# Optimization experiments

Measured on AMD Instinct MI355X. Metric: run time of the kernel, lower is better.

Reference implementation:

```python
import jax, jax.numpy as jnp
import numpy as np

NUM_USERS = 100000
NUM_ITEMS = 50000
EMBED_DIM = 64
NUM_LAYERS = 3
NNZ = 4800000  # 2 * num_interactions (symmetric bipartite adjacency)


def setup_inputs() -> dict:
    key = jax.random.key(0)
    k_u, k_i, k_r, k_c, k_v = jax.random.split(key, 5)
    N = NUM_USERS + NUM_ITEMS
    E = NNZ // 2
    # Xavier-uniform-style embeddings (any float init is fine for a math reference)
    user_emb = jax.random.normal(k_u, (NUM_USERS, EMBED_DIM), dtype=jnp.float32) * 0.1
    item_emb = jax.random.normal(k_i, (NUM_ITEMS, EMBED_DIM), dtype=jnp.float32) * 0.1
    # Build a symmetric bipartite COO adjacency: user->item and item->user edges.
    u = jax.random.randint(k_r, (E,), 0, NUM_USERS, dtype=jnp.int32)
    i = jax.random.randint(k_c, (E,), NUM_USERS, N, dtype=jnp.int32)
    adj_rows = jnp.concatenate([u, i])
    adj_cols = jnp.concatenate([i, u])
    # Normalized adjacency values (D^-1/2 A D^-1/2 in real LightGCN); random positive here.
    v = jax.random.uniform(k_v, (E,), dtype=jnp.float32, minval=0.01, maxval=0.1)
    adj_vals = jnp.concatenate([v, v])
    return {"user_emb": user_emb, "item_emb": item_emb, "adj_vals": adj_vals,
            "adj_rows": adj_rows, "adj_cols": adj_cols}


def reference(user_emb, item_emb, adj_vals, adj_rows, adj_cols):
    num_users = user_emb.shape[0]
    N = num_users + item_emb.shape[0]
    ego = jnp.concatenate([user_emb, item_emb], axis=0)  # [N, D]
    x = ego
    acc = ego  # running sum across layers (fused layer-mean)
    for _ in range(NUM_LAYERS):
        # SpMM: gather source embeddings, scale by edge value, scatter-add to rows.
        x = jax.ops.segment_sum(adj_vals[:, None] * x[adj_cols], adj_rows,
                                num_segments=N)
        acc = acc + x
    final = acc / jnp.asarray(NUM_LAYERS + 1, dtype=ego.dtype)
    return final[:num_users], final[num_users:]
```

## Files before the change

### kernel.cpp

```cpp
#include <hip/hip_runtime.h>

static constexpr int NUSERS = 100000;
static constexpr int NITEMS = 50000;
static constexpr int NNODES = NUSERS + NITEMS;
static constexpr int D      = 64;
static constexpr int NNZE   = 4800000;
static constexpr int NVEC4  = NNODES * D / 4;
static constexpr int NU4    = NUSERS * D / 4;

static constexpr int NB       = 512;
static constexpr int RPB      = (NNODES + NB - 1) / NB;
static constexpr int CHUNK    = 4096;
static constexpr int P1_BLOCKS = (NNZE + CHUNK - 1) / CHUNK;

__device__ __forceinline__ unsigned bf16rne(float f) {
    unsigned u = __float_as_uint(f);
    return (u + 0x7FFFu + ((u >> 16) & 1u)) >> 16;
}
__device__ __forceinline__ float bflo(unsigned u) { return __uint_as_float(u << 16); }
__device__ __forceinline__ float bfhi(unsigned u) { return __uint_as_float(u & 0xFFFF0000u); }

__global__ void lg_init(const float4* __restrict__ ue, const float4* __restrict__ ie,
                        uint2* __restrict__ x) {
    int stride = gridDim.x * blockDim.x;
    for (int i = blockIdx.x * blockDim.x + threadIdx.x; i < NVEC4; i += stride) {
        float4 v = (i < NU4) ? ue[i] : ie[i - NU4];
        x[i] = make_uint2(bf16rne(v.x) | (bf16rne(v.y) << 16),
                          bf16rne(v.z) | (bf16rne(v.w) << 16));
    }
}

__global__ void __launch_bounds__(512)
lg_bcnt(const int* __restrict__ rows, int* __restrict__ bucketCnt) {
    __shared__ int cnt[NB];
    int t = threadIdx.x;
    cnt[t] = 0;
    __syncthreads();
    int c0 = blockIdx.x * CHUNK;
    int c1 = min(c0 + CHUNK, NNZE);
    #pragma unroll
    for (int pass = 0; pass < 2; ++pass) {
        int e = c0 + (pass * 512 + t) * 4;
        if (e < c1) {
            int4 r4 = *(const int4*)(rows + e);
            atomicAdd(&cnt[r4.x / RPB], 1);
            atomicAdd(&cnt[r4.y / RPB], 1);
            atomicAdd(&cnt[r4.z / RPB], 1);
            atomicAdd(&cnt[r4.w / RPB], 1);
        }
    }
    __syncthreads();
    int n = cnt[t];
    if (n) atomicAdd(&bucketCnt[t], n);
}

__global__ void __launch_bounds__(512)
lg_bscan(const int* __restrict__ bucketCnt, int* __restrict__ bbase,
         int* __restrict__ gcur) {
    __shared__ int s[NB];
    int t = threadIdx.x;
    int v = bucketCnt[t];
    s[t] = v;
    __syncthreads();
    for (int off = 1; off < NB; off <<= 1) {
        int tmp = (t >= off) ? s[t - off] : 0;
        __syncthreads();
        s[t] += tmp;
        __syncthreads();
    }
    int ex = s[t] - v;
    bbase[t] = ex;
    gcur[t] = ex;
    if (t == NB - 1) bbase[NB] = s[t];
}

__global__ void __launch_bounds__(512)
lg_part1(const int* __restrict__ rows, const int* __restrict__ cols,
         const float* __restrict__ vals, int* __restrict__ gcur,
         int2* __restrict__ stage) {
    __shared__ int s_cnt[NB];
    __shared__ int s_lcur[NB];
    __shared__ int s_gofs[NB];
    __shared__ int2 s_pay[CHUNK];
    __shared__ unsigned short s_bid[CHUNK];
    int t = threadIdx.x;
    int c0 = blockIdx.x * CHUNK;
    int c1 = min(c0 + CHUNK, NNZE);
    s_cnt[t] = 0;
    __syncthreads();

    int  eb[8], ep[8]; float ev[8];
    bool has0, has1;
    {
        int e = c0 + t * 4;
        has0 = e < c1;
        if (has0) {
            int4 r4 = *(const int4*)(rows + e);
            int4 c4 = *(const int4*)(cols + e);
            float4 v4 = *(const float4*)(vals + e);
            eb[0] = r4.x / RPB; ep[0] = c4.x | ((r4.x - eb[0] * RPB) << 18); ev[0] = v4.x;
            eb[1] = r4.y / RPB; ep[1] = c4.y | ((r4.y - eb[1] * RPB) << 18); ev[1] = v4.y;
            eb[2] = r4.z / RPB; ep[2] = c4.z | ((r4.z - eb[2] * RPB) << 18); ev[2] = v4.z;
            eb[3] = r4.w / RPB; ep[3] = c4.w | ((r4.w - eb[3] * RPB) << 18); ev[3] = v4.w;
            atomicAdd(&s_cnt[eb[0]], 1); atomicAdd(&s_cnt[eb[1]], 1);
            atomicAdd(&s_cnt[eb[2]], 1); atomicAdd(&s_cnt[eb[3]], 1);
        }
        e = c0 + (512 + t) * 4;
        has1 = e < c1;
        if (has1) {
            int4 r4 = *(const int4*)(rows + e);
            int4 c4 = *(const int4*)(cols + e);
            float4 v4 = *(const float4*)(vals + e);
            eb[4] = r4.x / RPB; ep[4] = c4.x | ((r4.x - eb[4] * RPB) << 18); ev[4] = v4.x;
            eb[5] = r4.y / RPB; ep[5] = c4.y | ((r4.y - eb[5] * RPB) << 18); ev[5] = v4.y;
            eb[6] = r4.z / RPB; ep[6] = c4.z | ((r4.z - eb[6] * RPB) << 18); ev[6] = v4.z;
            eb[7] = r4.w / RPB; ep[7] = c4.w | ((r4.w - eb[7] * RPB) << 18); ev[7] = v4.w;
            atomicAdd(&s_cnt[eb[4]], 1); atomicAdd(&s_cnt[eb[5]], 1);
            atomicAdd(&s_cnt[eb[6]], 1); atomicAdd(&s_cnt[eb[7]], 1);
        }
    }
    __syncthreads();

    int myCnt = s_cnt[t];
    for (int off = 1; off < NB; off <<= 1) {
        int tmp = (t >= off) ? s_cnt[t - off] : 0;
        __syncthreads();
        s_cnt[t] += tmp;
        __syncthreads();
    }
    int lstart = s_cnt[t] - myCnt;
    int gbase = myCnt ? atomicAdd(&gcur[t], myCnt) : 0;
    s_lcur[t] = lstart;
    s_gofs[t] = gbase - lstart;
    __syncthreads();

    #pragma unroll
    for (int k = 0; k < 4; ++k) {
        if (has0) {
            int pos = atomicAdd(&s_lcur[eb[k]], 1);
            s_pay[pos] = make_int2(ep[k], __float_as_int(ev[k]));
            s_bid[pos] = (unsigned short)eb[k];
        }
    }
    #pragma unroll
    for (int k = 4; k < 8; ++k) {
        if (has1) {
            int pos = atomicAdd(&s_lcur[eb[k]], 1);
            s_pay[pos] = make_int2(ep[k], __float_as_int(ev[k]));
            s_bid[pos] = (unsigned short)eb[k];
        }
    }
    __syncthreads();

    int n = c1 - c0;
    for (int p = t; p < n; p += 512) {
        int b = s_bid[p];
        stage[s_gofs[b] + p] = s_pay[p];
    }
}

__global__ void __launch_bounds__(512)
lg_part2(const int* __restrict__ bbase, const int2* __restrict__ stage,
         int2* __restrict__ csr, int* __restrict__ rowptr) {
    __shared__ int s[NB];
    __shared__ int lcur[RPB];
    int b = blockIdx.x;
    int t = threadIdx.x;
    int r0 = b * RPB;
    int nrows = min(RPB, NNODES - r0);
    int s0 = bbase[b], s1 = bbase[b + 1];

    s[t] = 0;
    __syncthreads();
    for (int p = s0 + t; p < s1; p += 512)
        atomicAdd(&s[(stage[p].x >> 18) & 511], 1);
    __syncthreads();
    int v = s[t];
    for (int off = 1; off < NB; off <<= 1) {
        int tmp = (t >= off) ? s[t - off] : 0;
        __syncthreads();
        s[t] += tmp;
        __syncthreads();
    }
    int pos0 = s0 + s[t] - v;
    if (t < nrows) {
        rowptr[r0 + t] = pos0;
        lcur[t] = pos0;
    }
    if (b == gridDim.x - 1 && t == 0) rowptr[NNODES] = NNZE;
    __syncthreads();
    for (int p = s0 + t; p < s1; p += 512) {
        int2 cv = stage[p];
        int rl = (cv.x >> 18) & 511;
        int pos = atomicAdd(&lcur[rl], 1);
        csr[pos] = make_int2(cv.x & 0x3FFFF, cv.y);
    }
}

__global__ void __launch_bounds__(256)
lg_spmm(const int* __restrict__ rowptr, const int2* __restrict__ csr,
        const uint2* __restrict__ x, uint2* __restrict__ y) {
    int lane16 = threadIdx.x & 15;
    int r = (blockIdx.x * blockDim.x + threadIdx.x) >> 4;
    if (r >= NNODES) return;
    int p0 = rowptr[r], p1 = rowptr[r + 1];
    float4 acc = {0.f, 0.f, 0.f, 0.f};
    int p = p0;
    for (; p + 4 <= p1; p += 4) {
        int2 cv0 = csr[p], cv1 = csr[p + 1], cv2 = csr[p + 2], cv3 = csr[p + 3];
        uint2 x0 = x[cv0.x * 16 + lane16];
        uint2 x1 = x[cv1.x * 16 + lane16];
        uint2 x2 = x[cv2.x * 16 + lane16];
        uint2 x3 = x[cv3.x * 16 + lane16];
        float v0 = __int_as_float(cv0.y), v1 = __int_as_float(cv1.y);
        float v2 = __int_as_float(cv2.y), v3 = __int_as_float(cv3.y);
        acc.x += v0 * bflo(x0.x) + v1 * bflo(x1.x) + v2 * bflo(x2.x) + v3 * bflo(x3.x);
        acc.y += v0 * bfhi(x0.x) + v1 * bfhi(x1.x) + v2 * bfhi(x2.x) + v3 * bfhi(x3.x);
        acc.z += v0 * bflo(x0.y) + v1 * bflo(x1.y) + v2 * bflo(x2.y) + v3 * bflo(x3.y);
        acc.w += v0 * bfhi(x0.y) + v1 * bfhi(x1.y) + v2 * bfhi(x2.y) + v3 * bfhi(x3.y);
    }
    for (; p < p1; ++p) {
        int2 cv = csr[p];
        uint2 xv = x[cv.x * 16 + lane16];
        float v = __int_as_float(cv.y);
        acc.x += v * bflo(xv.x); acc.y += v * bfhi(xv.x);
        acc.z += v * bflo(xv.y); acc.w += v * bfhi(xv.y);
    }
    y[r * 16 + lane16] = make_uint2(bf16rne(acc.x) | (bf16rne(acc.y) << 16),
                                    bf16rne(acc.z) | (bf16rne(acc.w) << 16));
}

__global__ void lg_combine(const float4* __restrict__ ue, const float4* __restrict__ ie,
                           const uint2* __restrict__ y1, const uint2* __restrict__ y2,
                           const uint2* __restrict__ y3, float4* __restrict__ out) {
    int stride = gridDim.x * blockDim.x;
    for (int i = blockIdx.x * blockDim.x + threadIdx.x; i < NVEC4; i += stride) {
        float4 e = (i < NU4) ? ue[i] : ie[i - NU4];
        uint2 a = y1[i], b = y2[i], c = y3[i];
        float4 o;
        o.x = (e.x + bflo(a.x) + bflo(b.x) + bflo(c.x)) * 0.25f;
        o.y = (e.y + bfhi(a.x) + bfhi(b.x) + bfhi(c.x)) * 0.25f;
        o.z = (e.z + bflo(a.y) + bflo(b.y) + bflo(c.y)) * 0.25f;
        o.w = (e.w + bfhi(a.y) + bfhi(b.y) + bfhi(c.y)) * 0.25f;
        out[i] = o;
    }
}

extern "C" void kernel_launch(void* const* d_in, const int* in_sizes, int n_in,
                              void* d_out, int out_size, void* d_ws, size_t ws_size,
                              hipStream_t stream) {
    const float* ue   = (const float*)d_in[0];
    const float* ie   = (const float*)d_in[1];
    const float* vals = (const float*)d_in[2];
    const int*   rows = (const int*)d_in[3];
    const int*   cols = (const int*)d_in[4];
    float* out = (float*)d_out;

    uint2* xa     = (uint2*)d_ws;
    uint2* xb     = xa + NVEC4;
    int2*  csr    = (int2*)(xb + NVEC4);
    int2*  stage  = csr + NNZE;
    uint2* y3     = (uint2*)stage;
    int*   rowptr = (int*)(stage + NNZE);
    int*   bucketCnt = rowptr + (NNODES + 1);
    int*   bbase  = bucketCnt + NB;
    int*   gcur   = bbase + (NB + 1);

    const int spmmBlocks = NNODES * 16 / 256;

    lg_init<<<2048, 256, 0, stream>>>((const float4*)ue, (const float4*)ie, xa);
    hipMemsetAsync(bucketCnt, 0, NB * sizeof(int), stream);
    lg_bcnt<<<P1_BLOCKS, 512, 0, stream>>>(rows, bucketCnt);
    lg_bscan<<<1, NB, 0, stream>>>(bucketCnt, bbase, gcur);
    lg_part1<<<P1_BLOCKS, 512, 0, stream>>>(rows, cols, vals, gcur, stage);
    lg_part2<<<NB, 512, 0, stream>>>(bbase, stage, csr, rowptr);

    lg_spmm<<<spmmBlocks, 256, 0, stream>>>(rowptr, csr, xa, xb);
    lg_spmm<<<spmmBlocks, 256, 0, stream>>>(rowptr, csr, xb, xa);
    lg_spmm<<<spmmBlocks, 256, 0, stream>>>(rowptr, csr, xa, y3);

    lg_combine<<<2048, 256, 0, stream>>>((const float4*)ue, (const float4*)ie,
                                         xb, xa, y3, (float4*)out);
}
```

Measured before the change: 373.5 us.

## Split CSR into separate column and bf16 value arrays, unroll SpMM by eight

Edge values are rounded to bf16 during partitioning and stored as 16-bit values. The interleaved int2 staging and CSR arrays become a struct-of-arrays pair: a 4-byte column array and a 2-byte value array. This cuts per-edge metadata traffic from 8 to 6 bytes in the partition, sort and all three SpMM passes. The SpMM inner loop is also unrolled to 8 edges to keep more gathers in flight. The cost is extra precision loss on the adjacency weights and more separate loads per edge.

```diff
diff --git a/kernel.cpp b/kernel.cpp
--- a/kernel.cpp
+++ b/kernel.cpp
@@ -77,11 +77,12 @@
 __global__ void __launch_bounds__(512)
 lg_part1(const int* __restrict__ rows, const int* __restrict__ cols,
          const float* __restrict__ vals, int* __restrict__ gcur,
-         int2* __restrict__ stage) {
+         int* __restrict__ stagec, unsigned short* __restrict__ stagev) {
     __shared__ int s_cnt[NB];
     __shared__ int s_lcur[NB];
     __shared__ int s_gofs[NB];
-    __shared__ int2 s_pay[CHUNK];
+    __shared__ int s_payc[CHUNK];
+    __shared__ unsigned short s_payv[CHUNK];
     __shared__ unsigned short s_bid[CHUNK];
     int t = threadIdx.x;
     int c0 = blockIdx.x * CHUNK;
@@ -89,7 +90,7 @@
     s_cnt[t] = 0;
     __syncthreads();
 
-    int  eb[8], ep[8]; float ev[8];
+    int  eb[8], ep[8]; unsigned short ev[8];
     bool has0, has1;
     {
         int e = c0 + t * 4;
@@ -98,10 +99,10 @@
             int4 r4 = *(const int4*)(rows + e);
             int4 c4 = *(const int4*)(cols + e);
             float4 v4 = *(const float4*)(vals + e);
-            eb[0] = r4.x / RPB; ep[0] = c4.x | ((r4.x - eb[0] * RPB) << 18); ev[0] = v4.x;
-            eb[1] = r4.y / RPB; ep[1] = c4.y | ((r4.y - eb[1] * RPB) << 18); ev[1] = v4.y;
-            eb[2] = r4.z / RPB; ep[2] = c4.z | ((r4.z - eb[2] * RPB) << 18); ev[2] = v4.z;
-            eb[3] = r4.w / RPB; ep[3] = c4.w | ((r4.w - eb[3] * RPB) << 18); ev[3] = v4.w;
+            eb[0] = r4.x / RPB; ep[0] = c4.x | ((r4.x - eb[0] * RPB) << 18); ev[0] = (unsigned short)bf16rne(v4.x);
+            eb[1] = r4.y / RPB; ep[1] = c4.y | ((r4.y - eb[1] * RPB) << 18); ev[1] = (unsigned short)bf16rne(v4.y);
+            eb[2] = r4.z / RPB; ep[2] = c4.z | ((r4.z - eb[2] * RPB) << 18); ev[2] = (unsigned short)bf16rne(v4.z);
+            eb[3] = r4.w / RPB; ep[3] = c4.w | ((r4.w - eb[3] * RPB) << 18); ev[3] = (unsigned short)bf16rne(v4.w);
             atomicAdd(&s_cnt[eb[0]], 1); atomicAdd(&s_cnt[eb[1]], 1);
             atomicAdd(&s_cnt[eb[2]], 1); atomicAdd(&s_cnt[eb[3]], 1);
         }
@@ -111,10 +112,10 @@
             int4 r4 = *(const int4*)(rows + e);
             int4 c4 = *(const int4*)(cols + e);
             float4 v4 = *(const float4*)(vals + e);
-            eb[4] = r4.x / RPB; ep[4] = c4.x | ((r4.x - eb[4] * RPB) << 18); ev[4] = v4.x;
-            eb[5] = r4.y / RPB; ep[5] = c4.y | ((r4.y - eb[5] * RPB) << 18); ev[5] = v4.y;
-            eb[6] = r4.z / RPB; ep[6] = c4.z | ((r4.z - eb[6] * RPB) << 18); ev[6] = v4.z;
-            eb[7] = r4.w / RPB; ep[7] = c4.w | ((r4.w - eb[7] * RPB) << 18); ev[7] = v4.w;
+            eb[4] = r4.x / RPB; ep[4] = c4.x | ((r4.x - eb[4] * RPB) << 18); ev[4] = (unsigned short)bf16rne(v4.x);
+            eb[5] = r4.y / RPB; ep[5] = c4.y | ((r4.y - eb[5] * RPB) << 18); ev[5] = (unsigned short)bf16rne(v4.y);
+            eb[6] = r4.z / RPB; ep[6] = c4.z | ((r4.z - eb[6] * RPB) << 18); ev[6] = (unsigned short)bf16rne(v4.z);
+            eb[7] = r4.w / RPB; ep[7] = c4.w | ((r4.w - eb[7] * RPB) << 18); ev[7] = (unsigned short)bf16rne(v4.w);
             atomicAdd(&s_cnt[eb[4]], 1); atomicAdd(&s_cnt[eb[5]], 1);
             atomicAdd(&s_cnt[eb[6]], 1); atomicAdd(&s_cnt[eb[7]], 1);
         }
@@ -138,7 +139,8 @@
     for (int k = 0; k < 4; ++k) {
         if (has0) {
             int pos = atomicAdd(&s_lcur[eb[k]], 1);
-            s_pay[pos] = make_int2(ep[k], __float_as_int(ev[k]));
+            s_payc[pos] = ep[k];
+            s_payv[pos] = ev[k];
             s_bid[pos] = (unsigned short)eb[k];
         }
     }
@@ -146,7 +148,8 @@
     for (int k = 4; k < 8; ++k) {
         if (has1) {
             int pos = atomicAdd(&s_lcur[eb[k]], 1);
-            s_pay[pos] = make_int2(ep[k], __float_as_int(ev[k]));
+            s_payc[pos] = ep[k];
+            s_payv[pos] = ev[k];
             s_bid[pos] = (unsigned short)eb[k];
         }
     }
@@ -155,13 +158,17 @@
     int n = c1 - c0;
     for (int p = t; p < n; p += 512) {
         int b = s_bid[p];
-        stage[s_gofs[b] + p] = s_pay[p];
+        int dst = s_gofs[b] + p;
+        stagec[dst] = s_payc[p];
+        stagev[dst] = s_payv[p];
     }
 }
 
 __global__ void __launch_bounds__(512)
-lg_part2(const int* __restrict__ bbase, const int2* __restrict__ stage,
-         int2* __restrict__ csr, int* __restrict__ rowptr) {
+lg_part2(const int* __restrict__ bbase, const int* __restrict__ stagec,
+         const unsigned short* __restrict__ stagev,
+         int* __restrict__ csrc, unsigned short* __restrict__ csrv,
+         int* __restrict__ rowptr) {
     __shared__ int s[NB];
     __shared__ int lcur[RPB];
     int b = blockIdx.x;
@@ -173,7 +180,7 @@
     s[t] = 0;
     __syncthreads();
     for (int p = s0 + t; p < s1; p += 512)
-        atomicAdd(&s[(stage[p].x >> 18) & 511], 1);
+        atomicAdd(&s[(stagec[p] >> 18) & 511], 1);
     __syncthreads();
     int v = s[t];
     for (int off = 1; off < NB; off <<= 1) {
@@ -190,15 +197,18 @@
     if (b == gridDim.x - 1 && t == 0) rowptr[NNODES] = NNZE;
     __syncthreads();
     for (int p = s0 + t; p < s1; p += 512) {
-        int2 cv = stage[p];
-        int rl = (cv.x >> 18) & 511;
+        int pc = stagec[p];
+        unsigned short pv = stagev[p];
+        int rl = (pc >> 18) & 511;
         int pos = atomicAdd(&lcur[rl], 1);
-        csr[pos] = make_int2(cv.x & 0x3FFFF, cv.y);
+        csrc[pos] = pc & 0x3FFFF;
+        csrv[pos] = pv;
     }
 }
 
 __global__ void __launch_bounds__(256)
-lg_spmm(const int* __restrict__ rowptr, const int2* __restrict__ csr,
+lg_spmm(const int* __restrict__ rowptr, const int* __restrict__ csrc,
+        const unsigned short* __restrict__ csrv,
         const uint2* __restrict__ x, uint2* __restrict__ y) {
     int lane16 = threadIdx.x & 15;
     int r = (blockIdx.x * blockDim.x + threadIdx.x) >> 4;
@@ -206,23 +216,47 @@
     int p0 = rowptr[r], p1 = rowptr[r + 1];
     float4 acc = {0.f, 0.f, 0.f, 0.f};
     int p = p0;
+    for (; p + 8 <= p1; p += 8) {
+        int c0 = csrc[p],     c1 = csrc[p + 1], c2 = csrc[p + 2], c3 = csrc[p + 3];
+        int c4 = csrc[p + 4], c5 = csrc[p + 5], c6 = csrc[p + 6], c7 = csrc[p + 7];
+        unsigned short w0 = csrv[p],     w1 = csrv[p + 1], w2 = csrv[p + 2], w3 = csrv[p + 3];
+        unsigned short w4 = csrv[p + 4], w5 = csrv[p + 5], w6 = csrv[p + 6], w7 = csrv[p + 7];
+        uint2 x0 = x[c0 * 16 + lane16];
+        uint2 x1 = x[c1 * 16 + lane16];
+        uint2 x2 = x[c2 * 16 + lane16];
+        uint2 x3 = x[c3 * 16 + lane16];
+        uint2 x4 = x[c4 * 16 + lane16];
+        uint2 x5 = x[c5 * 16 + lane16];
+        uint2 x6 = x[c6 * 16 + lane16];
+        uint2 x7 = x[c7 * 16 + lane16];
+        float v0 = bflo(w0), v1 = bflo(w1), v2 = bflo(w2), v3 = bflo(w3);
+        float v4 = bflo(w4), v5 = bflo(w5), v6 = bflo(w6), v7 = bflo(w7);
+        acc.x += v0 * bflo(x0.x) + v1 * bflo(x1.x) + v2 * bflo(x2.x) + v3 * bflo(x3.x)
+               + v4 * bflo(x4.x) + v5 * bflo(x5.x) + v6 * bflo(x6.x) + v7 * bflo(x7.x);
+        acc.y += v0 * bfhi(x0.x) + v1 * bfhi(x1.x) + v2 * bfhi(x2.x) + v3 * bfhi(x3.x)
+               + v4 * bfhi(x4.x) + v5 * bfhi(x5.x) + v6 * bfhi(x6.x) + v7 * bfhi(x7.x);
+        acc.z += v0 * bflo(x0.y) + v1 * bflo(x1.y) + v2 * bflo(x2.y) + v3 * bflo(x3.y)
+               + v4 * bflo(x4.y) + v5 * bflo(x5.y) + v6 * bflo(x6.y) + v7 * bflo(x7.y);
+        acc.w += v0 * bfhi(x0.y) + v1 * bfhi(x1.y) + v2 * bfhi(x2.y) + v3 * bfhi(x3.y)
+               + v4 * bfhi(x4.y) + v5 * bfhi(x5.y) + v6 * bfhi(x6.y) + v7 * bfhi(x7.y);
+    }
     for (; p + 4 <= p1; p += 4) {
-        int2 cv0 = csr[p], cv1 = csr[p + 1], cv2 = csr[p + 2], cv3 = csr[p + 3];
-        uint2 x0 = x[cv0.x * 16 + lane16];
-        uint2 x1 = x[cv1.x * 16 + lane16];
-        uint2 x2 = x[cv2.x * 16 + lane16];
-        uint2 x3 = x[cv3.x * 16 + lane16];
-        float v0 = __int_as_float(cv0.y), v1 = __int_as_float(cv1.y);
-        float v2 = __int_as_float(cv2.y), v3 = __int_as_float(cv3.y);
+        int c0 = csrc[p], c1 = csrc[p + 1], c2 = csrc[p + 2], c3 = csrc[p + 3];
+        unsigned short w0 = csrv[p], w1 = csrv[p + 1], w2 = csrv[p + 2], w3 = csrv[p + 3];
+        uint2 x0 = x[c0 * 16 + lane16];
+        uint2 x1 = x[c1 * 16 + lane16];
+        uint2 x2 = x[c2 * 16 + lane16];
+        uint2 x3 = x[c3 * 16 + lane16];
+        float v0 = bflo(w0), v1 = bflo(w1), v2 = bflo(w2), v3 = bflo(w3);
         acc.x += v0 * bflo(x0.x) + v1 * bflo(x1.x) + v2 * bflo(x2.x) + v3 * bflo(x3.x);
         acc.y += v0 * bfhi(x0.x) + v1 * bfhi(x1.x) + v2 * bfhi(x2.x) + v3 * bfhi(x3.x);
         acc.z += v0 * bflo(x0.y) + v1 * bflo(x1.y) + v2 * bflo(x2.y) + v3 * bflo(x3.y);
         acc.w += v0 * bfhi(x0.y) + v1 * bfhi(x1.y) + v2 * bfhi(x2.y) + v3 * bfhi(x3.y);
     }
     for (; p < p1; ++p) {
-        int2 cv = csr[p];
-        uint2 xv = x[cv.x * 16 + lane16];
-        float v = __int_as_float(cv.y);
+        int c = csrc[p];
+        float v = bflo(csrv[p]);
+        uint2 xv = x[c * 16 + lane16];
         acc.x += v * bflo(xv.x); acc.y += v * bfhi(xv.x);
         acc.z += v * bflo(xv.y); acc.w += v * bfhi(xv.y);
     }
@@ -256,15 +290,17 @@
     const int*   cols = (const int*)d_in[4];
     float* out = (float*)d_out;
 
-    uint2* xa     = (uint2*)d_ws;
-    uint2* xb     = xa + NVEC4;
-    int2*  csr    = (int2*)(xb + NVEC4);
-    int2*  stage  = csr + NNZE;
-    uint2* y3     = (uint2*)stage;
-    int*   rowptr = (int*)(stage + NNZE);
-    int*   bucketCnt = rowptr + (NNODES + 1);
-    int*   bbase  = bucketCnt + NB;
-    int*   gcur   = bbase + (NB + 1);
+    uint2* xa             = (uint2*)d_ws;
+    uint2* xb             = xa + NVEC4;
+    int*   csrc           = (int*)(xb + NVEC4);
+    unsigned short* csrv  = (unsigned short*)(csrc + NNZE);
+    int*   stagec         = (int*)(csrv + NNZE);
+    unsigned short* stagev = (unsigned short*)(stagec + NNZE);
+    uint2* y3             = (uint2*)stagec;
+    int*   rowptr         = (int*)(stagev + NNZE);
+    int*   bucketCnt      = rowptr + (NNODES + 1);
+    int*   bbase          = bucketCnt + NB;
+    int*   gcur           = bbase + (NB + 1);
 
     const int spmmBlocks = NNODES * 16 / 256;
 
@@ -272,12 +308,12 @@
     hipMemsetAsync(bucketCnt, 0, NB * sizeof(int), stream);
     lg_bcnt<<<P1_BLOCKS, 512, 0, stream>>>(rows, bucketCnt);
     lg_bscan<<<1, NB, 0, stream>>>(bucketCnt, bbase, gcur);
-    lg_part1<<<P1_BLOCKS, 512, 0, stream>>>(rows, cols, vals, gcur, stage);
-    lg_part2<<<NB, 512, 0, stream>>>(bbase, stage, csr, rowptr);
-
-    lg_spmm<<<spmmBlocks, 256, 0, stream>>>(rowptr, csr, xa, xb);
-    lg_spmm<<<spmmBlocks, 256, 0, stream>>>(rowptr, csr, xb, xa);
-    lg_spmm<<<spmmBlocks, 256, 0, stream>>>(rowptr, csr, xa, y3);
+    lg_part1<<<P1_BLOCKS, 512, 0, stream>>>(rows, cols, vals, gcur, stagec, stagev);
+    lg_part2<<<NB, 512, 0, stream>>>(bbase, stagec, stagev, csrc, csrv, rowptr);
+
+    lg_spmm<<<spmmBlocks, 256, 0, stream>>>(rowptr, csrc, csrv, xa, xb);
+    lg_spmm<<<spmmBlocks, 256, 0, stream>>>(rowptr, csrc, csrv, xb, xa);
+    lg_spmm<<<spmmBlocks, 256, 0, stream>>>(rowptr, csrc, csrv, xa, y3);
 
     lg_combine<<<2048, 256, 0, stream>>>((const float4*)ue, (const float4*)ie,
                                          xb, xa, y3, (float4*)out);
```

New measurement: 387.4 us. +3.7%, slower.
